# Performance work log

Hardware: AMD Instinct MI355X
Metric: run time of the kernel (lower is better)

Reference implementation:

```python
import jax, jax.numpy as jnp
import numpy as np

EPS = 1e-6

def setup_inputs() -> dict:
    key = jax.random.key(0)
    k1, k2, k3, k4, k5 = jax.random.split(key, 5)
    B, Lq, Lk, D, Dc = 8, 1024, 8192, 256, 128
    q = jax.random.normal(k1, (B, Lq, D), dtype=jnp.float32)
    k_q = jax.random.randint(k2, (B, Lk, Dc), 0, 16, dtype=jnp.int32)  # 4-bit codes
    k_scale = jax.random.uniform(k3, (B, 1, Dc), dtype=jnp.float32)
    k_zero = jax.random.uniform(k4, (B, 1, Dc), dtype=jnp.float32) * 15.0
    W_up = jax.random.normal(k5, (D, Dc), dtype=jnp.float32) / np.sqrt(Dc)
    return {"q": q, "k_q": k_q, "k_scale": k_scale, "k_zero": k_zero, "W_up": W_up}

def reference(q, k_q, k_scale, k_zero, W_up):
    # int4 dequantization: (B, Lk, Dc)
    k_c = k_scale * (k_q.astype(jnp.float32) - k_zero)
    # low-rank decompress (nn.Linear(d_compressed, d_model, bias=False)): k = k_c @ W_up.T -> (B, Lk, D)
    k = jnp.einsum('blc,dc->bld', k_c, W_up)
    # squared norms (raw values used in diff, clamped values used in denominator)
    q_sq = jnp.sum(q * q, axis=-1)  # (B, Lq)
    k_sq = jnp.sum(k * k, axis=-1)  # (B, Lk)
    q_norm_sq = jnp.minimum(q_sq, 1.0 - EPS)
    k_norm_sq = jnp.minimum(k_sq, 1.0 - EPS)
    # ||q_i - k_j||^2 via expansion (same math as materializing the diff tensor)
    qk = jnp.einsum('bqd,bkd->bqk', q, k)  # (B, Lq, Lk)
    diff_norm_sq = jnp.maximum(q_sq[:, :, None] + k_sq[:, None, :] - 2.0 * qk, 0.0)
    denom = (1.0 - q_norm_sq)[:, :, None] * (1.0 - k_norm_sq)[:, None, :] + EPS
    dist = jnp.arccosh(1.0 + 2.0 * diff_norm_sq / denom)  # (B, Lq, Lk)
    return dist
```

## Files before the change

### kernel.cpp

```cpp
#include <hip/hip_runtime.h>
#include <hip/hip_bf16.h>

#define B_   8
#define LQ   1024
#define LK   8192
#define D_   256
#define DC   128
#define EPSF 1e-6f

typedef __attribute__((ext_vector_type(8))) short short8;
typedef __attribute__((ext_vector_type(4))) float floatx4;

static __device__ __forceinline__ floatx4 mfma16(short8 a, short8 b, floatx4 c) {
    return __builtin_amdgcn_mfma_f32_16x16x32_bf16(a, b, c, 0, 0, 0);
}
static __device__ __forceinline__ float fast_rcp(float x)  { return __builtin_amdgcn_rcpf(x); }
static __device__ __forceinline__ float fast_sqrt(float x) { return __builtin_amdgcn_sqrtf(x); }
static __device__ __forceinline__ float fast_ln(float x)   { return 0.69314718056f * __builtin_amdgcn_logf(x); }

static __device__ __forceinline__ void gl16(const void* g, void* l) {
    __builtin_amdgcn_global_load_lds(
        (const __attribute__((address_space(1))) unsigned int*)g,
        (__attribute__((address_space(3))) unsigned int*)l, 16, 0, 0);
}

__global__ __launch_bounds__(512) void k_G(const float* __restrict__ W,
                                           __hip_bfloat16* __restrict__ G,
                                           __hip_bfloat16* __restrict__ Wt) {
    __shared__ float red[512];
    int c1 = blockIdx.x;
    int t = threadIdx.x, c2 = t & 127, h = t >> 7;
    int d0 = h * 64;
    float a0 = 0.f, a1 = 0.f, a2 = 0.f, a3 = 0.f;
#pragma unroll 4
    for (int d = 0; d < 64; d += 4) {
        a0 += W[(size_t)(d0 + d + 0) * DC + c1] * W[(size_t)(d0 + d + 0) * DC + c2];
        a1 += W[(size_t)(d0 + d + 1) * DC + c1] * W[(size_t)(d0 + d + 1) * DC + c2];
        a2 += W[(size_t)(d0 + d + 2) * DC + c1] * W[(size_t)(d0 + d + 2) * DC + c2];
        a3 += W[(size_t)(d0 + d + 3) * DC + c1] * W[(size_t)(d0 + d + 3) * DC + c2];
    }
    red[t] = (a0 + a1) + (a2 + a3);
    if (t < 256) Wt[(size_t)c1 * D_ + t] = __float2bfloat16(W[(size_t)t * DC + c1]);
    __syncthreads();
    if (h == 0)
        G[c1 * DC + c2] =
            __float2bfloat16(red[c2] + red[128 + c2] + red[256 + c2] + red[384 + c2]);
}

static __device__ __forceinline__ void qproj_body(
        char* smem, int blk,
        const float* __restrict__ q, const __hip_bfloat16* __restrict__ Wt,
        __hip_bfloat16* __restrict__ qproj, float* __restrict__ q_sq) {
    __hip_bfloat16* sA = (__hip_bfloat16*)smem;
    __hip_bfloat16* sB = sA + 32 * 72;
    int t = threadIdx.x, lane = t & 63, w = t >> 6;
    int quad = lane >> 4, li = lane & 15;
    int wm = w >> 1, wn = w & 1;
    int row0 = blk * 32;

    float psum[2] = {0.f, 0.f};
    floatx4 acc[4];
#pragma unroll
    for (int nt = 0; nt < 4; ++nt) acc[nt] = (floatx4){0.f, 0.f, 0.f, 0.f};

    for (int kc4 = 0; kc4 < 4; ++kc4) {
#pragma unroll
        for (int it = 0; it < 2; ++it) {
            int idx = it * 256 + t;
            int r = idx >> 4, pos = idx & 15;
            float4 v = *(const float4*)(q + (size_t)(row0 + r) * D_ + kc4 * 64 + pos * 4);
            psum[it] += v.x * v.x + v.y * v.y + v.z * v.z + v.w * v.w;
            __hip_bfloat16* dst = &sA[r * 72 + pos * 4];
            dst[0] = __float2bfloat16(v.x); dst[1] = __float2bfloat16(v.y);
            dst[2] = __float2bfloat16(v.z); dst[3] = __float2bfloat16(v.w);
        }
#pragma unroll
        for (int it = 0; it < 4; ++it) {
            int e = it * 256 + t;
            int c = e >> 3, ch = e & 7;
            *(uint4*)&sB[c * 72 + ch * 8] =
                *(const uint4*)(Wt + (size_t)c * D_ + kc4 * 64 + ch * 8);
        }
        __syncthreads();
        short8 af[2];
#pragma unroll
        for (int ks = 0; ks < 2; ++ks)
            af[ks] = *(const short8*)&sA[(wm * 16 + li) * 72 + ks * 32 + quad * 8];
#pragma unroll
        for (int nt = 0; nt < 4; ++nt)
#pragma unroll
            for (int ks = 0; ks < 2; ++ks) {
                short8 bf = *(const short8*)&sB[((wn * 4 + nt) * 16 + li) * 72 + ks * 32 + quad * 8];
                acc[nt] = mfma16(af[ks], bf, acc[nt]);
            }
        __syncthreads();
    }
#pragma unroll
    for (int nt = 0; nt < 4; ++nt)
#pragma unroll
        for (int r = 0; r < 4; ++r) {
            int row = wm * 16 + quad * 4 + r;
            qproj[(size_t)(row0 + row) * DC + (wn * 4 + nt) * 16 + li] =
                __float2bfloat16(acc[nt][r]);
        }
#pragma unroll
    for (int it = 0; it < 2; ++it) {
        float s = psum[it];
        s += __shfl_xor(s, 1); s += __shfl_xor(s, 2);
        s += __shfl_xor(s, 4); s += __shfl_xor(s, 8);
        if (li == 0) q_sq[row0 + it * 16 + w * 4 + quad] = s;
    }
}

static __device__ __forceinline__ void dq_body(
        char* smem, int blk,
        const int* __restrict__ kq, const float* __restrict__ kscale,
        const float* __restrict__ kzero, const __hip_bfloat16* __restrict__ G,
        __hip_bfloat16* __restrict__ kc, float* __restrict__ k_sq) {
    __hip_bfloat16* sK = (__hip_bfloat16*)smem;
    int t = threadIdx.x, lane = t & 63, w = t >> 6;
    int quad = lane >> 4, li = lane & 15;
    int b = blk >> 7, l0 = (blk & 127) * 64;

    const int4* codes = (const int4*)(kq + ((size_t)b * LK + l0) * DC);
    int col = (t & 31) * 4;
    float4 sc = *(const float4*)(kscale + b * DC + col);
    float4 zp = *(const float4*)(kzero + b * DC + col);
    __hip_bfloat16* kco = kc + ((size_t)b * LK + l0) * DC;
#pragma unroll
    for (int it = 0; it < 8; ++it) {
        int idx = it * 256 + t;
        int r = idx >> 5;
        int4 c4 = codes[idx];
        __hip_bfloat16 tmp[4];
        tmp[0] = __float2bfloat16(sc.x * ((float)c4.x - zp.x));
        tmp[1] = __float2bfloat16(sc.y * ((float)c4.y - zp.y));
        tmp[2] = __float2bfloat16(sc.z * ((float)c4.z - zp.z));
        tmp[3] = __float2bfloat16(sc.w * ((float)c4.w - zp.w));
        *(uint2*)&sK[r * 132 + col] = *(const uint2*)tmp;
        *(uint2*)(kco + idx * 4)    = *(const uint2*)tmp;
    }
    __syncthreads();

    short8 af[4];
#pragma unroll
    for (int ks = 0; ks < 4; ++ks)
        af[ks] = *(const short8*)&sK[(w * 16 + li) * 132 + ks * 32 + quad * 8];
    float s4[4] = {0.f, 0.f, 0.f, 0.f};
#pragma unroll
    for (int nt = 0; nt < 8; ++nt) {
        floatx4 a0 = (floatx4){0.f, 0.f, 0.f, 0.f};
#pragma unroll
        for (int ks = 0; ks < 4; ++ks) {
            short8 bf = *(const short8*)(G + (size_t)(nt * 16 + li) * DC + ks * 32 + quad * 8);
            a0 = mfma16(af[ks], bf, a0);
        }
        int c2 = nt * 16 + li;
#pragma unroll
        for (int r = 0; r < 4; ++r)
            s4[r] += a0[r] * __bfloat162float(sK[(w * 16 + quad * 4 + r) * 132 + c2]);
    }
#pragma unroll
    for (int r = 0; r < 4; ++r) {
        float v = s4[r];
        v += __shfl_xor(v, 1); v += __shfl_xor(v, 2);
        v += __shfl_xor(v, 4); v += __shfl_xor(v, 8);
        if (li == 0)
            k_sq[(size_t)b * LK + l0 + w * 16 + quad * 4 + r] = v;
    }
}

__global__ __launch_bounds__(256) void k_prep(const float* __restrict__ q,
                                              const __hip_bfloat16* __restrict__ Wt,
                                              __hip_bfloat16* __restrict__ qproj,
                                              float* __restrict__ q_sq,
                                              const int* __restrict__ kq,
                                              const float* __restrict__ kscale,
                                              const float* __restrict__ kzero,
                                              const __hip_bfloat16* __restrict__ G,
                                              __hip_bfloat16* __restrict__ kc,
                                              float* __restrict__ k_sq) {
    __shared__ __align__(16) char smem[23040];
    if (blockIdx.x < 256)
        qproj_body(smem, blockIdx.x, q, Wt, qproj, q_sq);
    else
        dq_body(smem, blockIdx.x - 256, kq, kscale, kzero, G, kc, k_sq);
}

__global__ __launch_bounds__(256, 4) void k_main(const __hip_bfloat16* __restrict__ qproj,
                                                 const __hip_bfloat16* __restrict__ kc,
                                                 const float* __restrict__ q_sq,
                                                 const float* __restrict__ k_sq,
                                                 float* __restrict__ out) {
    __shared__ __align__(16) char smem[34816];
    __hip_bfloat16* sA = (__hip_bfloat16*)smem;
    __hip_bfloat16* sB = sA + 128 * 64;
    float* sO = (float*)smem;

    int t = threadIdx.x, lane = t & 63, w = t >> 6;
    int quad = lane >> 4, li = lane & 15;
    int wm = w >> 1, wn = w & 1;
    int blk = blockIdx.x;
    int b    = blk & 7;
    int rem0 = blk >> 3;
    int m0   = (rem0 & 7) << 7;
    int nt0  = rem0 >> 3;
    const char* Ag = (const char*)(qproj + ((size_t)b * LQ + m0) * DC);

    int lrow = lane >> 3;
    int lch  = (lane & 7) ^ lrow;

    int orow_t = t >> 4;
    int ocol4  = (t & 15) * 4;
    float qsA[8], omqA[8];
#pragma unroll
    for (int qq = 0; qq < 8; ++qq) {
        qsA[qq]  = q_sq[(size_t)b * LQ + m0 + qq * 16 + orow_t];
        omqA[qq] = 1.f - fminf(qsA[qq], 1.f - EPSF);
    }

    for (int s = 0; s < 4; ++s) {
        int n0 = (nt0 + s * 16) << 7;
        const char* Bg = (const char*)(kc + ((size_t)b * LK + n0) * DC);

        floatx4 acc[4][4];
#pragma unroll
        for (int i = 0; i < 4; ++i)
#pragma unroll
            for (int j = 0; j < 4; ++j)
                acc[i][j] = (floatx4){0.f, 0.f, 0.f, 0.f};

#pragma unroll
        for (int h = 0; h < 2; ++h) {
#pragma unroll
            for (int it = 0; it < 4; ++it) {
                int rbase = it * 32 + w * 8;
                size_t goff = (size_t)(rbase + lrow) * 256 + (size_t)(h * 8 + lch) * 16;
                gl16(Ag + goff, (char*)sA + rbase * 128);
                gl16(Bg + goff, (char*)sB + rbase * 128);
            }
            __syncthreads();
#pragma unroll
            for (int ks = 0; ks < 2; ++ks) {
                int ac = ((ks * 4 + quad) ^ (li & 7)) * 16;
                short8 qf[4], kf[4];
#pragma unroll
                for (int i = 0; i < 4; ++i) {
                    qf[i] = *(const short8*)((const char*)sA + (wm * 64 + i * 16 + li) * 128 + ac);
                    kf[i] = *(const short8*)((const char*)sB + (wn * 64 + i * 16 + li) * 128 + ac);
                }
#pragma unroll
                for (int i = 0; i < 4; ++i)
#pragma unroll
                    for (int j = 0; j < 4; ++j)
                        acc[i][j] = mfma16(kf[j], qf[i], acc[i][j]);
            }
            __syncthreads();
        }

#pragma unroll
        for (int p = 0; p < 2; ++p) {
#pragma unroll
            for (int jj = 0; jj < 2; ++jj) {
                int c = wn * 32 + jj * 16 + quad * 4;
#pragma unroll
                for (int i = 0; i < 4; ++i) {
                    int m = wm * 64 + i * 16 + li;
                    *(floatx4*)&sO[m * 68 + c] = acc[i][p * 2 + jj];
                }
            }
            __syncthreads();
            int nbase = (ocol4 >> 5) * 64 + p * 32 + (ocol4 & 31);
            floatx4 ks4 = *(const floatx4*)(k_sq + (size_t)b * LK + n0 + nbase);
            floatx4 kn;
#pragma unroll
            for (int r = 0; r < 4; ++r)
                kn[r] = 1.f - fminf(ks4[r], 1.f - EPSF);
#pragma unroll
            for (int qq = 0; qq < 8; ++qq) {
                int row = qq * 16 + orow_t;
                floatx4 v = *(const floatx4*)&sO[row * 68 + ocol4];
                float qs = qsA[qq], omq = omqA[qq];
                floatx4 o;
#pragma unroll
                for (int r = 0; r < 4; ++r) {
                    float diff  = fmaxf(qs + ks4[r] - 2.f * v[r], 0.f);
                    float delta = 2.f * diff * fast_rcp(omq * kn[r] + EPSF);
                    float sq    = fast_sqrt(delta * (delta + 2.f));
                    o[r] = fast_ln(1.f + delta + sq);
                }
                __builtin_nontemporal_store(
                    o, (floatx4*)(out + ((size_t)b * LQ + m0 + row) * (size_t)LK + n0 + nbase));
            }
            __syncthreads();
        }
    }
}

extern "C" void kernel_launch(void* const* d_in, const int* in_sizes, int n_in,
                              void* d_out, int out_size, void* d_ws, size_t ws_size,
                              hipStream_t stream) {
    const float* q      = (const float*)d_in[0];
    const int*   kq     = (const int*)d_in[1];
    const float* kscale = (const float*)d_in[2];
    const float* kzero  = (const float*)d_in[3];
    const float* W      = (const float*)d_in[4];
    float* out = (float*)d_out;

    char* ws = (char*)d_ws;
    __hip_bfloat16* qproj = (__hip_bfloat16*)(ws);
    __hip_bfloat16* kc    = (__hip_bfloat16*)(ws + 2097152);
    __hip_bfloat16* G     = (__hip_bfloat16*)(ws + 18874368);
    float*          q_sq  = (float*)(ws + 18907136);
    float*          k_sq  = (float*)(ws + 18939904);
    __hip_bfloat16* Wt    = (__hip_bfloat16*)out;

    k_G    <<<128, 512, 0, stream>>>(W, G, Wt);
    k_prep <<<1280, 256, 0, stream>>>(q, Wt, qproj, q_sq, kq, kscale, kzero, G, kc, k_sq);
    k_main <<<1024, 256, 0, stream>>>(qproj, kc, q_sq, k_sq, out);
}
```

Measured before the change: 361.3 us.

## Restructure main kernel: register-resident Q fragments, double-buffered K tiles, direct stores

The main distance kernel now holds a 32-row block of projected queries in registers for the whole K=128 reduction and streams 64-row tiles of the compressed keys through a double-buffered LDS pipeline with a single barrier per tile. The epilogue works directly on MFMA accumulators and stores output with no shared-memory transpose step, which removes several barriers and LDS round trips per tile. The costs are less data reuse per block (smaller M tile, so the keys are re-read for more query blocks) and output stores in 16-byte pieces per lane across rows, which may coalesce less well than the old row-contiguous pattern.

```diff
diff --git a/kernel.cpp b/kernel.cpp
--- a/kernel.cpp
+++ b/kernel.cpp
@@ -192,108 +192,87 @@
                                                  const float* __restrict__ q_sq,
                                                  const float* __restrict__ k_sq,
                                                  float* __restrict__ out) {
-    __shared__ __align__(16) char smem[34816];
-    __hip_bfloat16* sA = (__hip_bfloat16*)smem;
-    __hip_bfloat16* sB = sA + 128 * 64;
-    float* sO = (float*)smem;
-
+    __shared__ __align__(16) char smem[2 * 16384];
     int t = threadIdx.x, lane = t & 63, w = t >> 6;
     int quad = lane >> 4, li = lane & 15;
-    int wm = w >> 1, wn = w & 1;
     int blk = blockIdx.x;
-    int b    = blk & 7;
-    int rem0 = blk >> 3;
-    int m0   = (rem0 & 7) << 7;
-    int nt0  = rem0 >> 3;
-    const char* Ag = (const char*)(qproj + ((size_t)b * LQ + m0) * DC);
-
-    int lrow = lane >> 3;
-    int lch  = (lane & 7) ^ lrow;
-
-    int orow_t = t >> 4;
-    int ocol4  = (t & 15) * 4;
-    float qsA[8], omqA[8];
-#pragma unroll
-    for (int qq = 0; qq < 8; ++qq) {
-        qsA[qq]  = q_sq[(size_t)b * LQ + m0 + qq * 16 + orow_t];
-        omqA[qq] = 1.f - fminf(qsA[qq], 1.f - EPSF);
-    }
-
-    for (int s = 0; s < 4; ++s) {
-        int n0 = (nt0 + s * 16) << 7;
-        const char* Bg = (const char*)(kc + ((size_t)b * LK + n0) * DC);
-
-        floatx4 acc[4][4];
-#pragma unroll
-        for (int i = 0; i < 4; ++i)
-#pragma unroll
-            for (int j = 0; j < 4; ++j)
-                acc[i][j] = (floatx4){0.f, 0.f, 0.f, 0.f};
-
-#pragma unroll
-        for (int h = 0; h < 2; ++h) {
-#pragma unroll
-            for (int it = 0; it < 4; ++it) {
-                int rbase = it * 32 + w * 8;
-                size_t goff = (size_t)(rbase + lrow) * 256 + (size_t)(h * 8 + lch) * 16;
-                gl16(Ag + goff, (char*)sA + rbase * 128);
-                gl16(Bg + goff, (char*)sB + rbase * 128);
+    int b     = blk & 7;
+    int u     = blk >> 3;
+    int m0    = (u & 31) << 5;
+    int nbase = (u >> 5) << 11;
+
+    const char* kcb = (const char*)kc + ((size_t)b * LK) * 256;
+
+    short8 af[2][4];
+#pragma unroll
+    for (int mf = 0; mf < 2; ++mf)
+#pragma unroll
+        for (int ks = 0; ks < 4; ++ks)
+            af[mf][ks] = *(const short8*)((const char*)qproj
+                + ((size_t)b * LQ + m0 + mf * 16 + li) * 256 + ks * 64 + quad * 16);
+
+    float qs[2], omq[2];
+    float* orow[2];
+#pragma unroll
+    for (int mf = 0; mf < 2; ++mf) {
+        qs[mf]  = q_sq[(size_t)b * LQ + m0 + mf * 16 + li];
+        omq[mf] = 1.f - fminf(qs[mf], 1.f - EPSF);
+        orow[mf] = out + ((size_t)b * LQ + m0 + mf * 16 + li) * (size_t)LK;
+    }
+    const float* ksqb = k_sq + (size_t)b * LK;
+
+    int loff[4];
+#pragma unroll
+    for (int it = 0; it < 4; ++it) {
+        int sr = w * 16 + it * 4 + (lane >> 4);
+        loff[it] = sr * 256 + ((((lane & 15) ^ (sr & 7))) << 4);
+    }
+
+    auto stage = [&](int tile, int buf) {
+        size_t nb = ((size_t)(nbase + tile * 64)) << 8;
+        char* db = smem + (buf << 14);
+#pragma unroll
+        for (int it = 0; it < 4; ++it)
+            gl16(kcb + nb + loff[it], db + ((w * 16 + it * 4) << 8));
+    };
+
+    stage(0, 0);
+    __syncthreads();
+
+    for (int tl = 0; tl < 32; ++tl) {
+        if (tl + 1 < 32) stage(tl + 1, (tl + 1) & 1);
+
+        const char* sb = smem + ((tl & 1) << 14);
+        floatx4 acc[2];
+        acc[0] = (floatx4){0.f, 0.f, 0.f, 0.f};
+        acc[1] = (floatx4){0.f, 0.f, 0.f, 0.f};
+#pragma unroll
+        for (int ks = 0; ks < 4; ++ks) {
+            short8 bf = *(const short8*)(sb + (w * 16 + li) * 256
+                                         + ((((ks * 4 + quad) ^ (li & 7))) << 4));
+            acc[0] = mfma16(bf, af[0][ks], acc[0]);
+            acc[1] = mfma16(bf, af[1][ks], acc[1]);
+        }
+
+        int n_t = nbase + tl * 64 + w * 16 + quad * 4;
+        floatx4 k4 = *(const floatx4*)(ksqb + n_t);
+        floatx4 kn;
+#pragma unroll
+        for (int r = 0; r < 4; ++r)
+            kn[r] = 1.f - fminf(k4[r], 1.f - EPSF);
+#pragma unroll
+        for (int mf = 0; mf < 2; ++mf) {
+            floatx4 o;
+#pragma unroll
+            for (int r = 0; r < 4; ++r) {
+                float diff  = fmaxf(qs[mf] + k4[r] - 2.f * acc[mf][r], 0.f);
+                float delta = 2.f * diff * fast_rcp(omq[mf] * kn[r] + EPSF);
+                float sq    = fast_sqrt(delta * (delta + 2.f));
+                o[r] = fast_ln(1.f + delta + sq);
             }
-            __syncthreads();
-#pragma unroll
-            for (int ks = 0; ks < 2; ++ks) {
-                int ac = ((ks * 4 + quad) ^ (li & 7)) * 16;
-                short8 qf[4], kf[4];
-#pragma unroll
-                for (int i = 0; i < 4; ++i) {
-                    qf[i] = *(const short8*)((const char*)sA + (wm * 64 + i * 16 + li) * 128 + ac);
-                    kf[i] = *(const short8*)((const char*)sB + (wn * 64 + i * 16 + li) * 128 + ac);
-                }
-#pragma unroll
-                for (int i = 0; i < 4; ++i)
-#pragma unroll
-                    for (int j = 0; j < 4; ++j)
-                        acc[i][j] = mfma16(kf[j], qf[i], acc[i][j]);
-            }
-            __syncthreads();
-        }
-
-#pragma unroll
-        for (int p = 0; p < 2; ++p) {
-#pragma unroll
-            for (int jj = 0; jj < 2; ++jj) {
-                int c = wn * 32 + jj * 16 + quad * 4;
-#pragma unroll
-                for (int i = 0; i < 4; ++i) {
-                    int m = wm * 64 + i * 16 + li;
-                    *(floatx4*)&sO[m * 68 + c] = acc[i][p * 2 + jj];
-                }
-            }
-            __syncthreads();
-            int nbase = (ocol4 >> 5) * 64 + p * 32 + (ocol4 & 31);
-            floatx4 ks4 = *(const floatx4*)(k_sq + (size_t)b * LK + n0 + nbase);
-            floatx4 kn;
-#pragma unroll
-            for (int r = 0; r < 4; ++r)
-                kn[r] = 1.f - fminf(ks4[r], 1.f - EPSF);
-#pragma unroll
-            for (int qq = 0; qq < 8; ++qq) {
-                int row = qq * 16 + orow_t;
-                floatx4 v = *(const floatx4*)&sO[row * 68 + ocol4];
-                float qs = qsA[qq], omq = omqA[qq];
-                floatx4 o;
-#pragma unroll
-                for (int r = 0; r < 4; ++r) {
-                    float diff  = fmaxf(qs + ks4[r] - 2.f * v[r], 0.f);
-                    float delta = 2.f * diff * fast_rcp(omq * kn[r] + EPSF);
-                    float sq    = fast_sqrt(delta * (delta + 2.f));
-                    o[r] = fast_ln(1.f + delta + sq);
-                }
-                __builtin_nontemporal_store(
-                    o, (floatx4*)(out + ((size_t)b * LQ + m0 + row) * (size_t)LK + n0 + nbase));
-            }
-            __syncthreads();
-        }
+            __builtin_nontemporal_store(o, (floatx4*)(orow[mf] + n_t));
+        }
+        __syncthreads();
     }
 }
 
```

Measured after the change: 371.8 us. 1.03x slower.
